# Optimization experiments

Hardware: AMD Instinct MI355X
Metric: run time of the kernel (lower is better)

The kernel has to match this reference:

```python
import jax, jax.numpy as jnp
import numpy as np

N_FLOWS = 20
DIM = 4
BATCH = 8388608  # 2**23 samples -> 128 MB fp32 input


def setup_inputs() -> dict:
    key = jax.random.key(0)
    k1, k2, k3, k4 = jax.random.split(key, 4)
    return {
        "X": jax.random.normal(k1, (BATCH, DIM), dtype=jnp.float32),
        "x0s": jax.random.normal(k2, (N_FLOWS, DIM), dtype=jnp.float32),
        "alpha_primes": jax.random.normal(k3, (N_FLOWS,), dtype=jnp.float32),
        "beta_primes": jax.random.normal(k4, (N_FLOWS,), dtype=jnp.float32),
    }


def reference(X, x0s, alpha_primes, beta_primes):
    """Chain of 20 pyro-style Radial flow transforms on dim-4 vectors.

    Each flow: alpha = softplus(alpha'), beta = -alpha + softplus(beta')
               y = x + beta * (x - x0) / (alpha + ||x - x0||)
    """
    def step(x, params):
        x0, a_p, b_p = params
        alpha = jax.nn.softplus(a_p)                 # scalar > 0
        beta = -alpha + jax.nn.softplus(b_p)         # beta >= -alpha (invertibility)
        diff = x - x0                                # [B, 4]
        r = jnp.linalg.norm(diff, axis=-1, keepdims=True)  # [B, 1]
        return x + beta * diff / (alpha + r), None

    X, _ = jax.lax.scan(step, X, (x0s, alpha_primes, beta_primes))
    return X
```

## Files before the change

kernel.cpp:

```cpp
#include <hip/hip_runtime.h>

#define N_FLOWS 20
#define DIM 4
#define ITEMS 8
#define BLOCK 256

typedef float v2f __attribute__((ext_vector_type(2)));

__global__ void radial_setup(const float* __restrict__ x0s,
                             const float* __restrict__ alpha_primes,
                             const float* __restrict__ beta_primes,
                             float* __restrict__ ws) {
    int f = threadIdx.x;
    if (f < N_FLOWS) {
        float alpha = __logf(1.0f + __expf(alpha_primes[f]));
        float beta  = __logf(1.0f + __expf(beta_primes[f])) - alpha;
        float* p = ws + 8 * f;
        const bool last = (f == N_FLOWS - 1);
#pragma unroll
        for (int j = 0; j < 4; ++j)
            p[j] = x0s[4 * f + j] - (last ? 0.0f : x0s[4 * (f + 1) + j]);
        p[4] = alpha;
        p[5] = beta;
        p[6] = 0.0f;
        p[7] = 0.0f;
    } else if (f == N_FLOWS) {
        float* p = ws + 8 * N_FLOWS;
        p[0] = x0s[0]; p[1] = x0s[1]; p[2] = x0s[2]; p[3] = x0s[3];
        p[4] = 0.0f; p[5] = 0.0f; p[6] = 0.0f; p[7] = 0.0f;
    }
}

__global__ __launch_bounds__(BLOCK) void radial_main(
    const float4* __restrict__ Xv,
    const float4* __restrict__ P,
    float4* __restrict__ Ov)
{
    const unsigned base = blockIdx.x * (BLOCK * ITEMS) + threadIdx.x;

    float4 z = P[2 * N_FLOWS];
    v2f z01 = (v2f){z.x, z.y};
    v2f z23 = (v2f){z.z, z.w};

    v2f a[ITEMS], b[ITEMS];
#pragma unroll
    for (int i = 0; i < ITEMS; ++i) {
        float4 v = Xv[base + i * BLOCK];
        a[i] = (v2f){v.x, v.y} - z01;
        b[i] = (v2f){v.z, v.w} - z23;
    }

#pragma unroll
    for (int f = 0; f < N_FLOWS; ++f) {
        float4 c  = P[2 * f];
        float4 ab = P[2 * f + 1];
        v2f c01 = (v2f){c.x, c.y};
        v2f c23 = (v2f){c.z, c.w};
        float alpha = ab.x, beta = ab.y;
#pragma unroll
        for (int i = 0; i < ITEMS; ++i) {
            v2f q = a[i] * a[i];
            q += b[i] * b[i];
            float r2 = q.x + q.y;
            float r  = __builtin_amdgcn_sqrtf(r2);
            float s  = __builtin_fmaf(beta,
                                      __builtin_amdgcn_rcpf(alpha + r),
                                      1.0f);
            v2f sv = (v2f){s, s};
            a[i] = sv * a[i] + c01;
            b[i] = sv * b[i] + c23;
        }
    }

#pragma unroll
    for (int i = 0; i < ITEMS; ++i) {
        float4 v;
        v.x = a[i].x; v.y = a[i].y; v.z = b[i].x; v.w = b[i].y;
        Ov[base + i * BLOCK] = v;
    }
}

__global__ void radial_tail(const float4* __restrict__ Xv,
                            const float4* __restrict__ P,
                            float4* __restrict__ Ov,
                            int start, int batch)
{
    int idx = start + blockIdx.x * blockDim.x + threadIdx.x;
    if (idx >= batch) return;
    float4 z = P[2 * N_FLOWS];
    float4 v = Xv[idx];
    float dx = v.x - z.x, dy = v.y - z.y, dz = v.z - z.z, dw = v.w - z.w;
#pragma unroll
    for (int f = 0; f < N_FLOWS; ++f) {
        float4 c  = P[2 * f];
        float4 ab = P[2 * f + 1];
        float r2 = dx * dx + dy * dy + dz * dz + dw * dw;
        float r  = __builtin_amdgcn_sqrtf(r2);
        float s  = __builtin_fmaf(ab.y, __builtin_amdgcn_rcpf(ab.x + r), 1.0f);
        dx = s * dx + c.x; dy = s * dy + c.y;
        dz = s * dz + c.z; dw = s * dw + c.w;
    }
    float4 o; o.x = dx; o.y = dy; o.z = dz; o.w = dw;
    Ov[idx] = o;
}

extern "C" void kernel_launch(void* const* d_in, const int* in_sizes, int n_in,
                              void* d_out, int out_size, void* d_ws, size_t ws_size,
                              hipStream_t stream) {
    const float* X   = (const float*)d_in[0];
    const float* x0s = (const float*)d_in[1];
    const float* ap  = (const float*)d_in[2];
    const float* bp  = (const float*)d_in[3];
    float* out = (float*)d_out;
    float* ws  = (float*)d_ws;

    int batch = in_sizes[0] / DIM;

    radial_setup<<<1, 64, 0, stream>>>(x0s, ap, bp, ws);

    const int tile = BLOCK * ITEMS;
    int full_blocks = batch / tile;
    if (full_blocks > 0)
        radial_main<<<full_blocks, BLOCK, 0, stream>>>(
            (const float4*)X, (const float4*)ws, (float4*)out);

    int done = full_blocks * tile;
    int rem = batch - done;
    if (rem > 0)
        radial_tail<<<(rem + 255) / 256, 256, 0, stream>>>(
            (const float4*)X, (const float4*)ws, (float4*)out, done, batch);
}
```

Before: 243.9 us.

## Use persistent blocks with double-buffered prefetch and batched reciprocals in radial flows

Replaces the one-tile-per-block launch with a fixed grid of 2048 persistent blocks that each walk several tiles, prefetching the next tile's inputs into a second register buffer while computing the current one. Items per thread drop from 8 to 4 and launch bounds request 8 waves per SIMD. Within each flow the four per-item reciprocals are replaced by one reciprocal of their product plus multiplications (Montgomery batch inversion). The aim is to hide HBM latency and cut transcendental work. The cost is that the product of four denominators could overflow or lose precision, and occupancy now depends on register pressure.

```diff
diff --git a/kernel.cpp b/kernel.cpp
--- a/kernel.cpp
+++ b/kernel.cpp
@@ -2,8 +2,10 @@
 
 #define N_FLOWS 20
 #define DIM 4
-#define ITEMS 8
+#define ITEMS 4
 #define BLOCK 256
+#define PBLOCKS 2048
+#define TILE (BLOCK * ITEMS)
 
 typedef float v2f __attribute__((ext_vector_type(2)));
 
@@ -31,25 +33,8 @@
     }
 }
 
-__global__ __launch_bounds__(BLOCK) void radial_main(
-    const float4* __restrict__ Xv,
-    const float4* __restrict__ P,
-    float4* __restrict__ Ov)
-{
-    const unsigned base = blockIdx.x * (BLOCK * ITEMS) + threadIdx.x;
-
-    float4 z = P[2 * N_FLOWS];
-    v2f z01 = (v2f){z.x, z.y};
-    v2f z23 = (v2f){z.z, z.w};
-
-    v2f a[ITEMS], b[ITEMS];
-#pragma unroll
-    for (int i = 0; i < ITEMS; ++i) {
-        float4 v = Xv[base + i * BLOCK];
-        a[i] = (v2f){v.x, v.y} - z01;
-        b[i] = (v2f){v.z, v.w} - z23;
-    }
-
+__device__ __forceinline__ void flow_chain(v2f a[ITEMS], v2f b[ITEMS],
+                                           const float4* __restrict__ P) {
 #pragma unroll
     for (int f = 0; f < N_FLOWS; ++f) {
         float4 c  = P[2 * f];
@@ -57,34 +42,103 @@
         v2f c01 = (v2f){c.x, c.y};
         v2f c23 = (v2f){c.z, c.w};
         float alpha = ab.x, beta = ab.y;
+
+        float D[ITEMS];
 #pragma unroll
         for (int i = 0; i < ITEMS; ++i) {
             v2f q = a[i] * a[i];
             q += b[i] * b[i];
             float r2 = q.x + q.y;
-            float r  = __builtin_amdgcn_sqrtf(r2);
-            float s  = __builtin_fmaf(beta,
-                                      __builtin_amdgcn_rcpf(alpha + r),
-                                      1.0f);
+            D[i] = alpha + __builtin_amdgcn_sqrtf(r2);
+        }
+        float p1  = D[0] * D[1];
+        float p2  = p1 * D[2];
+        float p3  = p2 * D[3];
+        float inv = __builtin_amdgcn_rcpf(p3);
+        float i3 = inv * p2;
+        float w2 = inv * D[3];
+        float i2 = w2 * p1;
+        float w1 = w2 * D[2];
+        float i1 = w1 * D[0];
+        float i0 = w1 * D[1];
+        float invD[ITEMS] = {i0, i1, i2, i3};
+#pragma unroll
+        for (int i = 0; i < ITEMS; ++i) {
+            float s = __builtin_fmaf(beta, invD[i], 1.0f);
             v2f sv = (v2f){s, s};
             a[i] = sv * a[i] + c01;
             b[i] = sv * b[i] + c23;
         }
     }
+}
 
+__device__ __forceinline__ void compute_store(const float4 (&buf)[ITEMS],
+                                              unsigned idx, v2f z01, v2f z23,
+                                              const float4* __restrict__ P,
+                                              float4* __restrict__ Ov) {
+    v2f a[ITEMS], b[ITEMS];
+#pragma unroll
+    for (int i = 0; i < ITEMS; ++i) {
+        a[i] = (v2f){buf[i].x, buf[i].y} - z01;
+        b[i] = (v2f){buf[i].z, buf[i].w} - z23;
+    }
+    flow_chain(a, b, P);
 #pragma unroll
     for (int i = 0; i < ITEMS; ++i) {
         float4 v;
         v.x = a[i].x; v.y = a[i].y; v.z = b[i].x; v.w = b[i].y;
-        Ov[base + i * BLOCK] = v;
+        Ov[idx + i * BLOCK] = v;
+    }
+}
+
+__global__ __launch_bounds__(BLOCK, 8) void radial_main(
+    const float4* __restrict__ Xv,
+    const float4* __restrict__ P,
+    float4* __restrict__ Ov,
+    int T) {
+    float4 z = P[2 * N_FLOWS];
+    v2f z01 = (v2f){z.x, z.y};
+    v2f z23 = (v2f){z.z, z.w};
+
+    const unsigned tbase = (unsigned)blockIdx.x * (unsigned)T;
+    const unsigned lane  = threadIdx.x;
+
+    float4 A[ITEMS], B[ITEMS];
+    {
+        unsigned idx = tbase * TILE + lane;
+#pragma unroll
+        for (int i = 0; i < ITEMS; ++i) A[i] = Xv[idx + i * BLOCK];
+    }
+
+    int t = 0;
+    for (;;) {
+        {
+            unsigned idx = (tbase + t) * TILE + lane;
+            if (t + 1 < T) {
+                unsigned idn = idx + TILE;
+#pragma unroll
+                for (int i = 0; i < ITEMS; ++i) B[i] = Xv[idn + i * BLOCK];
+            }
+            compute_store(A, idx, z01, z23, P, Ov);
+        }
+        if (++t >= T) break;
+        {
+            unsigned idx = (tbase + t) * TILE + lane;
+            if (t + 1 < T) {
+                unsigned idn = idx + TILE;
+#pragma unroll
+                for (int i = 0; i < ITEMS; ++i) A[i] = Xv[idn + i * BLOCK];
+            }
+            compute_store(B, idx, z01, z23, P, Ov);
+        }
+        if (++t >= T) break;
     }
 }
 
 __global__ void radial_tail(const float4* __restrict__ Xv,
                             const float4* __restrict__ P,
                             float4* __restrict__ Ov,
-                            int start, int batch)
-{
+                            int start, int batch) {
     int idx = start + blockIdx.x * blockDim.x + threadIdx.x;
     if (idx >= batch) return;
     float4 z = P[2 * N_FLOWS];
@@ -115,16 +169,22 @@
     float* ws  = (float*)d_ws;
 
     int batch = in_sizes[0] / DIM;
+    int tiles = batch / TILE;
 
     radial_setup<<<1, 64, 0, stream>>>(x0s, ap, bp, ws);
 
-    const int tile = BLOCK * ITEMS;
-    int full_blocks = batch / tile;
-    if (full_blocks > 0)
-        radial_main<<<full_blocks, BLOCK, 0, stream>>>(
-            (const float4*)X, (const float4*)ws, (float4*)out);
+    int done = 0;
+    if (tiles >= PBLOCKS) {
+        int T = tiles / PBLOCKS;
+        radial_main<<<PBLOCKS, BLOCK, 0, stream>>>(
+            (const float4*)X, (const float4*)ws, (float4*)out, T);
+        done = PBLOCKS * T * TILE;
+    } else if (tiles > 0) {
+        radial_main<<<tiles, BLOCK, 0, stream>>>(
+            (const float4*)X, (const float4*)ws, (float4*)out, 1);
+        done = tiles * TILE;
+    }
 
-    int done = full_blocks * tile;
     int rem = batch - done;
     if (rem > 0)
         radial_tail<<<(rem + 255) / 256, 256, 0, stream>>>(
```

New measurement: 255.5 us. 4.8% more time.

## Use persistent blocks with double-buffered tile loads and batched reciprocal

Applied to the files above, without the earlier changes.

Replaces the one-tile-per-block launch with 1024 persistent blocks that each walk several tiles of 4 items per thread. The next tile's loads are issued before the current tile is computed, so memory latency is hidden behind compute. Per flow, the four reciprocals are merged into a single rcp using the product trick (Montgomery batch inversion), and outputs are written with nontemporal stores. This costs extra multiplies and more register pressure, and the shared reciprocal can overflow or underflow when the product of denominators is extreme.

```diff
diff --git a/kernel.cpp b/kernel.cpp
--- a/kernel.cpp
+++ b/kernel.cpp
@@ -2,10 +2,13 @@
 
 #define N_FLOWS 20
 #define DIM 4
-#define ITEMS 8
+#define ITEMS 4
 #define BLOCK 256
+#define PBLOCKS 1024
+#define TILE (BLOCK * ITEMS)
 
 typedef float v2f __attribute__((ext_vector_type(2)));
+typedef float v4f __attribute__((ext_vector_type(4)));
 
 __global__ void radial_setup(const float* __restrict__ x0s,
                              const float* __restrict__ alpha_primes,
@@ -31,60 +34,106 @@
     }
 }
 
-__global__ __launch_bounds__(BLOCK) void radial_main(
+
+#define LOADT(V0, V1, V2, V3, IDXV)               \
+    do {                                          \
+        V0 = Xv[(IDXV)];                          \
+        V1 = Xv[(IDXV) + BLOCK];                  \
+        V2 = Xv[(IDXV) + 2 * BLOCK];              \
+        V3 = Xv[(IDXV) + 3 * BLOCK];              \
+    } while (0)
+
+#define COMPSTORE(V0, V1, V2, V3, IDXV)                                        \
+    do {                                                                       \
+        v2f a0 = (v2f){V0.x, V0.y} - z01;                                      \
+        v2f b0 = (v2f){V0.z, V0.w} - z23;                                      \
+        v2f a1 = (v2f){V1.x, V1.y} - z01;                                      \
+        v2f b1 = (v2f){V1.z, V1.w} - z23;                                      \
+        v2f a2 = (v2f){V2.x, V2.y} - z01;                                      \
+        v2f b2 = (v2f){V2.z, V2.w} - z23;                                      \
+        v2f a3 = (v2f){V3.x, V3.y} - z01;                                      \
+        v2f b3 = (v2f){V3.z, V3.w} - z23;                                      \
+        _Pragma("unroll")                                                      \
+        for (int f = 0; f < N_FLOWS; ++f) {                                    \
+            float4 c  = P[2 * f];                       \
+            float4 ab = P[2 * f + 1];                                          \
+            v2f c01 = (v2f){c.x, c.y};                                         \
+            v2f c23 = (v2f){c.z, c.w};                                         \
+            float alpha = ab.x, beta = ab.y;                                   \
+            v2f q0 = a0 * a0; q0 += b0 * b0;                                   \
+            v2f q1 = a1 * a1; q1 += b1 * b1;                                   \
+            v2f q2 = a2 * a2; q2 += b2 * b2;                                   \
+            v2f q3 = a3 * a3; q3 += b3 * b3;                                   \
+            float D0 = alpha + __builtin_amdgcn_sqrtf(q0.x + q0.y);            \
+            float D1 = alpha + __builtin_amdgcn_sqrtf(q1.x + q1.y);            \
+            float D2 = alpha + __builtin_amdgcn_sqrtf(q2.x + q2.y);            \
+            float D3 = alpha + __builtin_amdgcn_sqrtf(q3.x + q3.y);            \
+            float p1  = D0 * D1;                                               \
+            float p2  = p1 * D2;                                               \
+            float p3  = p2 * D3;                                               \
+            float inv = __builtin_amdgcn_rcpf(p3);                             \
+            float i3 = inv * p2;                                     \
+            float w2 = inv * D3;                             \
+            float i2 = w2 * p1;                                      \
+            float w1 = w2 * D2;                                 \
+            float i1 = w1 * D0;                                      \
+            float i0 = w1 * D1;                                      \
+            float s0 = __builtin_fmaf(beta, i0, 1.0f);                         \
+            float s1 = __builtin_fmaf(beta, i1, 1.0f);                         \
+            float s2 = __builtin_fmaf(beta, i2, 1.0f);                         \
+            float s3 = __builtin_fmaf(beta, i3, 1.0f);                         \
+            v2f sv;                                                            \
+            sv = (v2f){s0, s0}; a0 = sv * a0 + c01; b0 = sv * b0 + c23;        \
+            sv = (v2f){s1, s1}; a1 = sv * a1 + c01; b1 = sv * b1 + c23;        \
+            sv = (v2f){s2, s2}; a2 = sv * a2 + c01; b2 = sv * b2 + c23;        \
+            sv = (v2f){s3, s3}; a3 = sv * a3 + c01; b3 = sv * b3 + c23;        \
+        }                                                                      \
+        v4f o;                                                                 \
+        o = (v4f){a0.x, a0.y, b0.x, b0.y};                                     \
+        __builtin_nontemporal_store(o, Ovv + (IDXV));                          \
+        o = (v4f){a1.x, a1.y, b1.x, b1.y};                                     \
+        __builtin_nontemporal_store(o, Ovv + (IDXV) + BLOCK);                  \
+        o = (v4f){a2.x, a2.y, b2.x, b2.y};                                     \
+        __builtin_nontemporal_store(o, Ovv + (IDXV) + 2 * BLOCK);              \
+        o = (v4f){a3.x, a3.y, b3.x, b3.y};                                     \
+        __builtin_nontemporal_store(o, Ovv + (IDXV) + 3 * BLOCK);              \
+    } while (0)
+
+__global__ __launch_bounds__(BLOCK, 4) void radial_main(
     const float4* __restrict__ Xv,
     const float4* __restrict__ P,
-    float4* __restrict__ Ov)
+    float4* __restrict__ Ov,
+    int T)
 {
-    const unsigned base = blockIdx.x * (BLOCK * ITEMS) + threadIdx.x;
+    v4f* __restrict__ Ovv = (v4f*)Ov;
 
     float4 z = P[2 * N_FLOWS];
     v2f z01 = (v2f){z.x, z.y};
     v2f z23 = (v2f){z.z, z.w};
 
-    v2f a[ITEMS], b[ITEMS];
-#pragma unroll
-    for (int i = 0; i < ITEMS; ++i) {
-        float4 v = Xv[base + i * BLOCK];
-        a[i] = (v2f){v.x, v.y} - z01;
-        b[i] = (v2f){v.z, v.w} - z23;
-    }
+    const unsigned lane = threadIdx.x;
+    unsigned idx = (unsigned)blockIdx.x * (unsigned)T * TILE + lane;
 
-#pragma unroll
-    for (int f = 0; f < N_FLOWS; ++f) {
-        float4 c  = P[2 * f];
-        float4 ab = P[2 * f + 1];
-        v2f c01 = (v2f){c.x, c.y};
-        v2f c23 = (v2f){c.z, c.w};
-        float alpha = ab.x, beta = ab.y;
-#pragma unroll
-        for (int i = 0; i < ITEMS; ++i) {
-            v2f q = a[i] * a[i];
-            q += b[i] * b[i];
-            float r2 = q.x + q.y;
-            float r  = __builtin_amdgcn_sqrtf(r2);
-            float s  = __builtin_fmaf(beta,
-                                      __builtin_amdgcn_rcpf(alpha + r),
-                                      1.0f);
-            v2f sv = (v2f){s, s};
-            a[i] = sv * a[i] + c01;
-            b[i] = sv * b[i] + c23;
-        }
-    }
+    float4 A0, A1, A2, A3, B0, B1, B2, B3;
 
-#pragma unroll
-    for (int i = 0; i < ITEMS; ++i) {
-        float4 v;
-        v.x = a[i].x; v.y = a[i].y; v.z = b[i].x; v.w = b[i].y;
-        Ov[base + i * BLOCK] = v;
+    LOADT(A0, A1, A2, A3, idx);
+    int t = 0;
+    for (;;) {
+        if (t + 1 < T) LOADT(B0, B1, B2, B3, idx + TILE);
+        COMPSTORE(A0, A1, A2, A3, idx);
+        if (++t >= T) break;
+        idx += TILE;
+        if (t + 1 < T) LOADT(A0, A1, A2, A3, idx + TILE);
+        COMPSTORE(B0, B1, B2, B3, idx);
+        if (++t >= T) break;
+        idx += TILE;
     }
 }
 
 __global__ void radial_tail(const float4* __restrict__ Xv,
                             const float4* __restrict__ P,
                             float4* __restrict__ Ov,
-                            int start, int batch)
-{
+                            int start, int batch) {
     int idx = start + blockIdx.x * blockDim.x + threadIdx.x;
     if (idx >= batch) return;
     float4 z = P[2 * N_FLOWS];
@@ -115,16 +164,22 @@
     float* ws  = (float*)d_ws;
 
     int batch = in_sizes[0] / DIM;
+    int tiles = batch / TILE;
 
     radial_setup<<<1, 64, 0, stream>>>(x0s, ap, bp, ws);
 
-    const int tile = BLOCK * ITEMS;
-    int full_blocks = batch / tile;
-    if (full_blocks > 0)
-        radial_main<<<full_blocks, BLOCK, 0, stream>>>(
-            (const float4*)X, (const float4*)ws, (float4*)out);
+    int done = 0;
+    if (tiles >= PBLOCKS) {
+        int T = tiles / PBLOCKS;
+        radial_main<<<PBLOCKS, BLOCK, 0, stream>>>(
+            (const float4*)X, (const float4*)ws, (float4*)out, T);
+        done = PBLOCKS * T * TILE;
+    } else if (tiles > 0) {
+        radial_main<<<tiles, BLOCK, 0, stream>>>(
+            (const float4*)X, (const float4*)ws, (float4*)out, 1);
+        done = tiles * TILE;
+    }
 
-    int done = full_blocks * tile;
     int rem = batch - done;
     if (rem > 0)
         radial_tail<<<(rem + 255) / 256, 256, 0, stream>>>(
```

Result: slower. 254.2 us (+4.2%).
